# Optimization experiments

Hardware: AMD Instinct MI355X
Metric: run time of the kernel (lower is better)

The kernel has to match this reference:

```python
import jax, jax.numpy as jnp
import numpy as np

N_NODES = 100000
N_EDGES = 3200000
IN_DIM, H_DIM, OUT_DIM = 512, 256, 128
NEG_SLOPE = 0.25


def setup_inputs() -> dict:
    key = jax.random.key(0)
    ks = jax.random.split(key, 8)
    x = jax.random.normal(ks[0], (N_NODES, IN_DIM), dtype=jnp.float32)
    # xavier-normal-ish init for weights, zero bias (matches module init)
    W1 = jax.random.normal(ks[1], (IN_DIM, H_DIM), dtype=jnp.float32) * np.sqrt(2.0 / (IN_DIM + H_DIM))
    b1 = jnp.zeros((H_DIM,), dtype=jnp.float32)
    W2 = jax.random.normal(ks[2], (H_DIM, OUT_DIM), dtype=jnp.float32) * np.sqrt(2.0 / (H_DIM + OUT_DIM))
    b2 = jnp.zeros((OUT_DIM,), dtype=jnp.float32)
    adj_row = jax.random.randint(ks[3], (N_EDGES,), 0, N_NODES, dtype=jnp.int32)
    adj_col = jax.random.randint(ks[4], (N_EDGES,), 0, N_NODES, dtype=jnp.int32)
    # positive normalized-ish edge weights (like D^-1/2 A D^-1/2 entries)
    edge_weight = jax.random.uniform(ks[5], (N_EDGES,), dtype=jnp.float32) * 0.05
    return {"x": x, "W1": W1, "b1": b1, "W2": W2, "b2": b2,
            "adj_row": adj_row, "adj_col": adj_col, "edge_weight": edge_weight}


def reference(x, W1, b1, W2, b2, adj_row, adj_col, edge_weight):
    n = x.shape[0]

    def spmm(support):
        # out[r] = sum over edges (r, c): w * support[c]   (COO SpMM)
        msgs = edge_weight[:, None] * support[adj_col]  # [E, d] gather
        return jax.ops.segment_sum(msgs, adj_row, num_segments=n)

    def leaky(h):
        return jnp.where(h > 0, h, NEG_SLOPE * h)

    h = leaky(spmm(x @ W1) + b1)          # gc1 + leaky_relu (dropout = eval mode)
    h = leaky(spmm(h @ W2) + b2)          # gc2 + leaky_relu
    return h
```

## Files before the change

### kernel.cpp

```cpp
#include <hip/hip_runtime.h>

typedef unsigned short u16;
typedef unsigned char u8;
typedef __attribute__((ext_vector_type(8))) __bf16 bf16x8;
typedef __attribute__((ext_vector_type(4))) float f32x4;

#define CAP   4608
#define CHUNK 8192
#define NBKT_PAD 800

static __device__ __forceinline__ u16 f2bf(float f) {
    unsigned u = __float_as_uint(f);
    u += 0x7fffu + ((u >> 16) & 1u);
    return (u16)(u >> 16);
}
static __device__ __forceinline__ float bf2f(u16 v) {
    return __uint_as_float(((unsigned)v) << 16);
}
static __device__ __forceinline__ void gl_lds16(const void* g, void* l) {
    __builtin_amdgcn_global_load_lds((const __attribute__((address_space(1))) void*)g,
                                     (__attribute__((address_space(3))) void*)l, 16, 0, 0);
}


__global__ __launch_bounds__(256) void bucket_k(const int* __restrict__ row,
                                                const int* __restrict__ col,
                                                const float* __restrict__ w,
                                                int* __restrict__ gcount,
                                                int2* __restrict__ edges, int E) {
    __shared__ int hist[NBKT_PAD];
    __shared__ int lscan[NBKT_PAD];
    __shared__ int lcnt[NBKT_PAD];
    __shared__ int gbase[NBKT_PAD];
    __shared__ int tsum[256];
    __shared__ int2 pay[CHUNK];
    __shared__ int  dst[CHUNK];
    const int base = blockIdx.x * CHUNK;
    const int cntC = min(CHUNK, E - base);
    const int tid = threadIdx.x;

    for (int i = tid; i < NBKT_PAD; i += 256) { hist[i] = 0; lcnt[i] = 0; }
    __syncthreads();

    for (int i = tid; i < cntC; i += 256) atomicAdd(&hist[row[base + i] >> 7], 1);
    __syncthreads();

    int h[4], s = 0;
    #pragma unroll
    for (int j = 0; j < 4; ++j) {
        int bb = tid * 4 + j;
        h[j] = (bb < NBKT_PAD) ? hist[bb] : 0;
        s += h[j];
    }
    tsum[tid] = s;
    __syncthreads();
    for (int d = 1; d < 256; d <<= 1) {
        int t = (tid >= d) ? tsum[tid - d] : 0;
        __syncthreads();
        tsum[tid] += t;
        __syncthreads();
    }
    int run = tsum[tid] - s;
    #pragma unroll
    for (int j = 0; j < 4; ++j) {
        int bb = tid * 4 + j;
        if (bb < NBKT_PAD) {
            lscan[bb] = run;
            run += h[j];
            if (h[j] > 0) gbase[bb] = atomicAdd(&gcount[bb], h[j]);
        }
    }
    __syncthreads();

    for (int i = tid; i < cntC; i += 256) {
        int r = row[base + i];
        int c = col[base + i];
        float ww = w[base + i];
        int bb = r >> 7;
        int lp = atomicAdd(&lcnt[bb], 1);
        int slot = lscan[bb] + lp;
        int pos = gbase[bb] + lp;
        pay[slot] = make_int2(((r & 127) << 17) | c, __float_as_int(ww));
        dst[slot] = (pos < CAP) ? bb * CAP + pos : -1;
    }
    __syncthreads();

    for (int i = tid; i < cntC; i += 256) {
        int d = dst[i];
        if (d >= 0) edges[d] = pay[i];
    }
}


__global__ __launch_bounds__(256) void rsort_k(const int* __restrict__ gcount,
                                               int2* __restrict__ edges,
                                               int2* __restrict__ rc, int n) {
    __shared__ int2 pay[CAP];
    __shared__ int2 pay2[CAP];
    __shared__ int hist[128];
    __shared__ int sc[128];
    __shared__ int lcnt[128];
    const int b = blockIdx.x, tid = threadIdx.x;
    const int cnt = min(gcount[b], CAP);
    int2* eb = edges + (size_t)b * CAP;

    if (tid < 128) { hist[tid] = 0; lcnt[tid] = 0; }
    __syncthreads();

    for (int i = tid; i < cnt; i += 256) {
        int2 e = eb[i];
        pay[i] = e;
        atomicAdd(&hist[((unsigned)e.x) >> 17], 1);
    }
    __syncthreads();

    int h = (tid < 128) ? hist[tid] : 0;
    if (tid < 128) sc[tid] = h;
    __syncthreads();
    for (int d = 1; d < 128; d <<= 1) {
        int t = 0;
        if (tid < 128 && tid >= d) t = sc[tid - d];
        __syncthreads();
        if (tid < 128) sc[tid] += t;
        __syncthreads();
    }
    if (tid < 128) {
        sc[tid] -= h;
        int gr = b * 128 + tid;
        if (gr < n) rc[gr] = make_int2(b * CAP + sc[tid], h);
    }
    __syncthreads();

    for (int i = tid; i < cnt; i += 256) {
        int2 e = pay[i];
        int rr = ((unsigned)e.x) >> 17;
        int slot = sc[rr] + atomicAdd(&lcnt[rr], 1);
        pay2[slot] = e;
    }
    __syncthreads();

    for (int i = tid; i < cnt; i += 256) eb[i] = pay2[i];
}


__global__ __launch_bounds__(256) void cvt_x(const float* __restrict__ x,
                                             u16* __restrict__ xb, long total) {
    long i = ((long)blockIdx.x * 256 + threadIdx.x) * 8;
    const long stride = (long)gridDim.x * 2048;
    for (; i < total; i += stride) {
        float4 f0 = *(const float4*)(x + i);
        float4 f1 = *(const float4*)(x + i + 4);
        alignas(16) u16 t[8];
        t[0] = f2bf(f0.x); t[1] = f2bf(f0.y); t[2] = f2bf(f0.z); t[3] = f2bf(f0.w);
        t[4] = f2bf(f1.x); t[5] = f2bf(f1.y); t[6] = f2bf(f1.z); t[7] = f2bf(f1.w);
        *(int4*)(xb + i) = *(const int4*)t;
    }
}


__global__ void transpose_w2(const float* __restrict__ W1, u16* __restrict__ W1T,
                             const float* __restrict__ W2, u16* __restrict__ W2T) {
    const int T1 = 512 * 256;
    const int T2 = 256 * 128;
    int i = blockIdx.x * blockDim.x + threadIdx.x;
    if (i < T1) {
        int k = i / 256, nn = i % 256;
        W1T[nn * 512 + k] = f2bf(W1[i]);
    } else if (i < T1 + T2) {
        int j = i - T1;
        int k = j / 128, nn = j % 128;
        W2T[nn * 256 + k] = f2bf(W2[j]);
    }
}


template <int K, int NWN>
__global__ void gemm_fq(const u16* __restrict__ A,
                        const u16* __restrict__ BT,
                        u8* __restrict__ supq,
                        float* __restrict__ scales, int M) {
    constexpr int BN = NWN * 64;
    constexpr int THREADS = NWN * 128;
    constexpr int A_ISS = 8192 / (THREADS * 16);
    constexpr int B_ISS = (BN * 64) / (THREADS * 16);
    constexpr int LOGN = (NWN == 4) ? 2 : 1;
    __shared__ alignas(16) u16 As[128 * 32];
    __shared__ alignas(16) u16 Bs[BN * 32];
    __shared__ float rmax[128][NWN];
    __shared__ u8 qtile[128 * BN];

    const int tid = threadIdx.x;
    const int lane = tid & 63, wv = tid >> 6;
    const int wm = wv >> LOGN, wn = wv & (NWN - 1);
    const int lr = lane & 15, lg = lane >> 4;
    const int mblk = blockIdx.x;
    f32x4 acc[4][4] = {};

    const u16* gA[A_ISS];
    const u16* gB[B_ISS];
    u16* lA[A_ISS];
    u16* lB[B_ISS];
    #pragma unroll
    for (int i = 0; i < A_ISS; ++i) {
        int t8 = i * THREADS + tid;
        long r = (long)mblk * 128 + (t8 >> 2);
        if (r >= M) r = M - 1;
        gA[i] = A + r * K + (t8 & 3) * 8;
        lA[i] = As + i * THREADS * 8 + wv * 512;
    }
    #pragma unroll
    for (int i = 0; i < B_ISS; ++i) {
        int t8 = i * THREADS + tid;
        gB[i] = BT + (long)(t8 >> 2) * K + (t8 & 3) * 8;
        lB[i] = Bs + i * THREADS * 8 + wv * 512;
    }

    #pragma unroll 2
    for (int kt = 0; kt < K; kt += 32) {
        #pragma unroll
        for (int i = 0; i < A_ISS; ++i) gl_lds16(gA[i] + kt, lA[i]);
        #pragma unroll
        for (int i = 0; i < B_ISS; ++i) gl_lds16(gB[i] + kt, lB[i]);
        __syncthreads();

        bf16x8 a[4], b[4];
        #pragma unroll
        for (int mi = 0; mi < 4; ++mi)
            a[mi] = *(const bf16x8*)&As[(wm * 64 + mi * 16 + lr) * 32 + lg * 8];
        #pragma unroll
        for (int ni = 0; ni < 4; ++ni)
            b[ni] = *(const bf16x8*)&Bs[(wn * 64 + ni * 16 + lr) * 32 + lg * 8];
        #pragma unroll
        for (int mi = 0; mi < 4; ++mi)
            #pragma unroll
            for (int ni = 0; ni < 4; ++ni)
                acc[mi][ni] = __builtin_amdgcn_mfma_f32_16x16x32_bf16(a[mi], b[ni], acc[mi][ni], 0, 0, 0);
        __syncthreads();
    }

    #pragma unroll
    for (int mi = 0; mi < 4; ++mi) {
        #pragma unroll
        for (int j = 0; j < 4; ++j) {
            float m = 0.f;
            #pragma unroll
            for (int ni = 0; ni < 4; ++ni) m = fmaxf(m, fabsf(acc[mi][ni][j]));
            m = fmaxf(m, __shfl_xor(m, 1));
            m = fmaxf(m, __shfl_xor(m, 2));
            m = fmaxf(m, __shfl_xor(m, 4));
            m = fmaxf(m, __shfl_xor(m, 8));
            if (lr == 0) rmax[wm * 64 + mi * 16 + lg * 4 + j][wn] = m;
        }
    }
    __syncthreads();

    #pragma unroll
    for (int mi = 0; mi < 4; ++mi) {
        #pragma unroll
        for (int j = 0; j < 4; ++j) {
            const int rl = wm * 64 + mi * 16 + lg * 4 + j;
            float m = rmax[rl][0];
            #pragma unroll
            for (int w2 = 1; w2 < NWN; ++w2) m = fmaxf(m, rmax[rl][w2]);
            const float inv = (m > 0.f) ? 127.f / m : 0.f;
            #pragma unroll
            for (int ni = 0; ni < 4; ++ni) {
                int q = (int)rintf(acc[mi][ni][j] * inv) + 128;
                qtile[rl * BN + wn * 64 + ni * 16 + lr] = (u8)q;
            }
        }
    }
    if (tid < 128) {
        int gr = mblk * 128 + tid;
        if (gr < M) {
            float m = rmax[tid][0];
            #pragma unroll
            for (int w2 = 1; w2 < NWN; ++w2) m = fmaxf(m, rmax[tid][w2]);
            scales[gr] = m * (1.f / 127.f);
        }
    }
    __syncthreads();

    constexpr int CHUNKS = (128 * BN) / (THREADS * 16);
    #pragma unroll
    for (int cc = 0; cc < CHUNKS; ++cc) {
        int off = cc * THREADS * 16 + tid * 16;
        int gr = mblk * 128 + off / BN;
        if (gr < M)
            *(int4*)(supq + (size_t)mblk * 128 * BN + off) = *(const int4*)&qtile[off];
    }
}


template <int D, bool OUT_BF16>
__global__ __launch_bounds__(256) void spmm_q(const int2* __restrict__ rc,
                                              const int2* __restrict__ edges,
                                              const u8* __restrict__ supq,
                                              const float* __restrict__ scales,
                                              const float* __restrict__ bias,
                                              u16* __restrict__ obf,
                                              float* __restrict__ of32, int n) {
    const int r = blockIdx.x * 4 + (threadIdx.x >> 6);
    if (r >= n) return;
    const int lane = threadIdx.x & 63;
    constexpr int V = D / 64;
    float acc[V];
    #pragma unroll
    for (int j = 0; j < V; ++j) acc[j] = 0.f;
    float kk = 0.f;

    const int2 se0 = rc[r];
    const int e0  = __builtin_amdgcn_readfirstlane(se0.x);
    const int cnt = __builtin_amdgcn_readfirstlane(se0.y);
    const int2* __restrict__ eb = edges + e0;
    const int loff = lane * V;

    int i = 0;
    for (; i + 4 <= cnt; i += 4) {
        int2 e[4];
        #pragma unroll
        for (int j = 0; j < 4; ++j) e[j] = eb[i + j];
        int c[4], sw[4];
        #pragma unroll
        for (int j = 0; j < 4; ++j) {
            c[j]  = __builtin_amdgcn_readfirstlane(e[j].x) & 0x1FFFF;
            sw[j] = __builtin_amdgcn_readfirstlane(e[j].y);
        }
        float s[4];
        #pragma unroll
        for (int j = 0; j < 4; ++j) s[j] = scales[c[j]];
        unsigned uv[4];
        #pragma unroll
        for (int j = 0; j < 4; ++j)
            uv[j] = *(const unsigned*)(supq + (size_t)c[j] * D + loff);
        float ws[4];
        #pragma unroll
        for (int j = 0; j < 4; ++j) ws[j] = __int_as_float(sw[j]) * s[j];
        #pragma unroll
        for (int j = 0; j < 4; ++j) {
            kk += ws[j];
            acc[0] += ws[j] * (float)(uv[j] & 0xFF);
            acc[1] += ws[j] * (float)((uv[j] >> 8) & 0xFF);
            if constexpr (V == 4) {
                acc[2] += ws[j] * (float)((uv[j] >> 16) & 0xFF);
                acc[3] += ws[j] * (float)(uv[j] >> 24);
            }
        }
    }
    for (; i < cnt; ++i) {
        int2 e = eb[i];
        int c  = __builtin_amdgcn_readfirstlane(e.x) & 0x1FFFF;
        int sw = __builtin_amdgcn_readfirstlane(e.y);
        float ws = __int_as_float(sw) * scales[c];
        unsigned uv = *(const unsigned*)(supq + (size_t)c * D + loff);
        kk += ws;
        acc[0] += ws * (float)(uv & 0xFF);
        acc[1] += ws * (float)((uv >> 8) & 0xFF);
        if constexpr (V == 4) {
            acc[2] += ws * (float)((uv >> 16) & 0xFF);
            acc[3] += ws * (float)(uv >> 24);
        }
    }

    const float off = 128.f * kk;
    if constexpr (V == 4) {
        const float4 bb = *(const float4*)&bias[lane * 4];
        float h0 = acc[0] - off + bb.x, h1 = acc[1] - off + bb.y;
        float h2 = acc[2] - off + bb.z, h3 = acc[3] - off + bb.w;
        h0 = h0 > 0.f ? h0 : 0.25f * h0;
        h1 = h1 > 0.f ? h1 : 0.25f * h1;
        h2 = h2 > 0.f ? h2 : 0.25f * h2;
        h3 = h3 > 0.f ? h3 : 0.25f * h3;
        const size_t o = (size_t)r * D + lane * 4;
        if constexpr (OUT_BF16) {
            ushort4 hv; hv.x = f2bf(h0); hv.y = f2bf(h1); hv.z = f2bf(h2); hv.w = f2bf(h3);
            *(ushort4*)&obf[o] = hv;
        } else {
            *(float4*)&of32[o] = make_float4(h0, h1, h2, h3);
        }
    } else {
        const float2 bb = *(const float2*)&bias[lane * 2];
        float h0 = acc[0] - off + bb.x, h1 = acc[1] - off + bb.y;
        h0 = h0 > 0.f ? h0 : 0.25f * h0;
        h1 = h1 > 0.f ? h1 : 0.25f * h1;
        const size_t o = (size_t)r * D + lane * 2;
        if constexpr (OUT_BF16) {
            ushort2 hv; hv.x = f2bf(h0); hv.y = f2bf(h1);
            *(ushort2*)&obf[o] = hv;
        } else {
            *(float2*)&of32[o] = make_float2(h0, h1);
        }
    }
}


extern "C" void kernel_launch(void* const* d_in, const int* in_sizes, int n_in,
                              void* d_out, int out_size, void* d_ws, size_t ws_size,
                              hipStream_t stream) {
    const float* x  = (const float*)d_in[0];
    const float* W1 = (const float*)d_in[1];
    const float* b1 = (const float*)d_in[2];
    const float* W2 = (const float*)d_in[3];
    const float* b2 = (const float*)d_in[4];
    const int* arow = (const int*)d_in[5];
    const int* acol = (const int*)d_in[6];
    const float* ew = (const float*)d_in[7];

    const int IN = 512, H = 256, OUT = 128;
    const int n = in_sizes[0] / IN;
    const int E = in_sizes[5];
    const int nbkt = (n + 127) >> 7;

    char* base = (char*)d_ws;
    size_t off = 0;
    auto carve = [&](size_t bytes) -> void* {
        void* r = base + off;
        off = (off + bytes + 255) & ~(size_t)255;
        return r;
    };
    int*   gcount = (int*)carve((size_t)NBKT_PAD * 4);
    int2*  edges  = (int2*)carve((size_t)nbkt * CAP * 8);
    int2*  rc     = (int2*)carve((size_t)n * 8);
    u16*   W1T    = (u16*)carve((size_t)H * IN * 2);
    u16*   W2T    = (u16*)carve((size_t)OUT * H * 2);
    u8*    supq   = (u8*)carve((size_t)n * H);
    float* scales = (float*)carve((size_t)n * 4);
    u16*   xb     = (u16*)carve((size_t)n * IN * 2);
    u16*   h1     = xb;

    hipMemsetAsync(gcount, 0, (size_t)NBKT_PAD * 4, stream);
    bucket_k<<<(E + CHUNK - 1) / CHUNK, 256, 0, stream>>>(arow, acol, ew, gcount, edges, E);
    rsort_k<<<nbkt, 256, 0, stream>>>(gcount, edges, rc, n);

    transpose_w2<<<(512 * 256 + 256 * 128 + 255) / 256, 256, 0, stream>>>(W1, W1T, W2, W2T);
    cvt_x<<<2048, 256, 0, stream>>>(x, xb, (long)n * IN);

    gemm_fq<512, 4><<<(n + 127) / 128, 512, 0, stream>>>(xb, W1T, supq, scales, n);
    spmm_q<256, true><<<(n + 3) / 4, 256, 0, stream>>>(rc, edges, supq, scales, b1, h1, nullptr, n);

    gemm_fq<256, 2><<<(n + 127) / 128, 256, 0, stream>>>(h1, W2T, supq, scales, n);
    spmm_q<128, false><<<(n + 3) / 4, 256, 0, stream>>>(rc, edges, supq, scales, b2, nullptr, (float*)d_out, n);
}
```

Before: 506.6 us.

## Split edges into SoA column-banded CSR, prescale weights, fuse x conversion into GEMM

The row-sort kernel now orders each row's edges by column band and writes separate column and weight arrays, padding each row to a multiple of four with zero-weight edges. A new pass multiplies each edge weight by the per-node quantization scale, so the SpMM does vector loads of four edges and software-pipelines its gathers without a dependent scale lookup. The standalone fp32-to-bf16 conversion of x is removed: the first GEMM now loads fp32 A tiles directly and converts them in registers. The costs are extra pre-scale kernels, padded storage, and register-path A loads in the GEMM in place of direct global-to-LDS loads.

```diff
diff --git a/kernel.cpp b/kernel.cpp
--- a/kernel.cpp
+++ b/kernel.cpp
@@ -6,8 +6,10 @@
 typedef __attribute__((ext_vector_type(4))) float f32x4;
 
 #define CAP   4608
+#define CAPO  5120
 #define CHUNK 8192
 #define NBKT_PAD 800
+#define NBAND 32
 
 static __device__ __forceinline__ u16 f2bf(float f) {
     unsigned u = __float_as_uint(f);
@@ -93,29 +95,38 @@
 
 
 __global__ __launch_bounds__(256) void rsort_k(const int* __restrict__ gcount,
-                                               int2* __restrict__ edges,
+                                               const int2* __restrict__ edges,
+                                               int* __restrict__ colsO,
+                                               float* __restrict__ wO,
                                                int2* __restrict__ rc, int n) {
-    __shared__ int2 pay[CAP];
-    __shared__ int2 pay2[CAP];
-    __shared__ int hist[128];
+    __shared__ int cnt2[128 * NBAND];
+    __shared__ int base2[128 * NBAND];
+    __shared__ int colsL[CAPO];
+    __shared__ float wL[CAPO];
     __shared__ int sc[128];
-    __shared__ int lcnt[128];
     const int b = blockIdx.x, tid = threadIdx.x;
     const int cnt = min(gcount[b], CAP);
-    int2* eb = edges + (size_t)b * CAP;
-
-    if (tid < 128) { hist[tid] = 0; lcnt[tid] = 0; }
+    const int2* eb = edges + (size_t)b * CAP;
+
+    for (int i = tid; i < 128 * NBAND; i += 256) cnt2[i] = 0;
+    for (int i = tid; i < CAPO; i += 256) { colsL[i] = 0; wL[i] = 0.f; }
     __syncthreads();
 
     for (int i = tid; i < cnt; i += 256) {
         int2 e = eb[i];
-        pay[i] = e;
-        atomicAdd(&hist[((unsigned)e.x) >> 17], 1);
-    }
-    __syncthreads();
-
-    int h = (tid < 128) ? hist[tid] : 0;
-    if (tid < 128) sc[tid] = h;
+        int rr = ((unsigned)e.x) >> 17;
+        int cc = e.x & 0x1FFFF;
+        atomicAdd(&cnt2[rr * NBAND + (cc >> 12)], 1);
+    }
+    __syncthreads();
+
+    int rtot = 0;
+    if (tid < 128) {
+        #pragma unroll
+        for (int bb = 0; bb < NBAND; ++bb) rtot += cnt2[tid * NBAND + bb];
+        rtot = (rtot + 3) & ~3;
+        sc[tid] = rtot;
+    }
     __syncthreads();
     for (int d = 1; d < 128; d <<= 1) {
         int t = 0;
@@ -125,35 +136,49 @@
         __syncthreads();
     }
     if (tid < 128) {
-        sc[tid] -= h;
+        int start = sc[tid] - rtot;
         int gr = b * 128 + tid;
-        if (gr < n) rc[gr] = make_int2(b * CAP + sc[tid], h);
+        if (gr < n) rc[gr] = make_int2(b * CAPO + start, rtot);
+        int run = start;
+        #pragma unroll
+        for (int bb = 0; bb < NBAND; ++bb) {
+            base2[tid * NBAND + bb] = run;
+            run += cnt2[tid * NBAND + bb];
+        }
     }
     __syncthreads();
 
     for (int i = tid; i < cnt; i += 256) {
-        int2 e = pay[i];
+        int2 e = eb[i];
         int rr = ((unsigned)e.x) >> 17;
-        int slot = sc[rr] + atomicAdd(&lcnt[rr], 1);
-        pay2[slot] = e;
-    }
-    __syncthreads();
-
-    for (int i = tid; i < cnt; i += 256) eb[i] = pay2[i];
-}
-
-
-__global__ __launch_bounds__(256) void cvt_x(const float* __restrict__ x,
-                                             u16* __restrict__ xb, long total) {
-    long i = ((long)blockIdx.x * 256 + threadIdx.x) * 8;
-    const long stride = (long)gridDim.x * 2048;
+        int cc = e.x & 0x1FFFF;
+        int slot = atomicAdd(&base2[rr * NBAND + (cc >> 12)], 1);
+        colsL[slot] = cc;
+        wL[slot] = __int_as_float(e.y);
+    }
+    __syncthreads();
+
+    int* co = colsO + (size_t)b * CAPO;
+    float* wo = wO + (size_t)b * CAPO;
+    for (int i = tid; i < CAPO; i += 256) { co[i] = colsL[i]; wo[i] = wL[i]; }
+}
+
+
+__global__ __launch_bounds__(256) void wscale_k(const int* __restrict__ cols,
+                                                const float* __restrict__ wr,
+                                                const float* __restrict__ scales,
+                                                float* __restrict__ ws, int total) {
+    int i = (blockIdx.x * 256 + threadIdx.x) * 4;
+    const int stride = gridDim.x * 1024;
     for (; i < total; i += stride) {
-        float4 f0 = *(const float4*)(x + i);
-        float4 f1 = *(const float4*)(x + i + 4);
-        alignas(16) u16 t[8];
-        t[0] = f2bf(f0.x); t[1] = f2bf(f0.y); t[2] = f2bf(f0.z); t[3] = f2bf(f0.w);
-        t[4] = f2bf(f1.x); t[5] = f2bf(f1.y); t[6] = f2bf(f1.z); t[7] = f2bf(f1.w);
-        *(int4*)(xb + i) = *(const int4*)t;
+        int4 c = *(const int4*)(cols + i);
+        float4 w = *(const float4*)(wr + i);
+        float4 o;
+        o.x = w.x * scales[c.x];
+        o.y = w.y * scales[c.y];
+        o.z = w.z * scales[c.z];
+        o.w = w.w * scales[c.w];
+        *(float4*)(ws + i) = o;
     }
 }
 
@@ -174,8 +199,8 @@
 }
 
 
-template <int K, int NWN>
-__global__ void gemm_fq(const u16* __restrict__ A,
+template <int K, int NWN, bool AF32>
+__global__ void gemm_fq(const void* __restrict__ Ap,
                         const u16* __restrict__ BT,
                         u8* __restrict__ supq,
                         float* __restrict__ scales, int M) {
@@ -183,6 +208,7 @@
     constexpr int THREADS = NWN * 128;
     constexpr int A_ISS = 8192 / (THREADS * 16);
     constexpr int B_ISS = (BN * 64) / (THREADS * 16);
+    constexpr int A_CH = 4096 / (THREADS * 8);
     constexpr int LOGN = (NWN == 4) ? 2 : 1;
     __shared__ alignas(16) u16 As[128 * 32];
     __shared__ alignas(16) u16 Bs[BN * 32];
@@ -195,19 +221,34 @@
     const int lr = lane & 15, lg = lane >> 4;
     const int mblk = blockIdx.x;
     f32x4 acc[4][4] = {};
-
-    const u16* gA[A_ISS];
+    const float* Af = (const float*)Ap;
+    const u16* Ab = (const u16*)Ap;
+
+    const u16* gA[A_ISS > 0 ? A_ISS : 1];
+    u16* lA[A_ISS > 0 ? A_ISS : 1];
+    const float* gAf[A_CH > 0 ? A_CH : 1];
+    u16* lAf[A_CH > 0 ? A_CH : 1];
+    if constexpr (AF32) {
+        #pragma unroll
+        for (int i = 0; i < A_CH; ++i) {
+            int t8 = i * THREADS + tid;
+            long r = (long)mblk * 128 + (t8 >> 2);
+            if (r >= M) r = M - 1;
+            gAf[i] = Af + r * K + (t8 & 3) * 8;
+            lAf[i] = As + (t8 >> 2) * 32 + (t8 & 3) * 8;
+        }
+    } else {
+        #pragma unroll
+        for (int i = 0; i < A_ISS; ++i) {
+            int t8 = i * THREADS + tid;
+            long r = (long)mblk * 128 + (t8 >> 2);
+            if (r >= M) r = M - 1;
+            gA[i] = Ab + r * K + (t8 & 3) * 8;
+            lA[i] = As + i * THREADS * 8 + wv * 512;
+        }
+    }
     const u16* gB[B_ISS];
-    u16* lA[A_ISS];
     u16* lB[B_ISS];
-    #pragma unroll
-    for (int i = 0; i < A_ISS; ++i) {
-        int t8 = i * THREADS + tid;
-        long r = (long)mblk * 128 + (t8 >> 2);
-        if (r >= M) r = M - 1;
-        gA[i] = A + r * K + (t8 & 3) * 8;
-        lA[i] = As + i * THREADS * 8 + wv * 512;
-    }
     #pragma unroll
     for (int i = 0; i < B_ISS; ++i) {
         int t8 = i * THREADS + tid;
@@ -217,8 +258,20 @@
 
     #pragma unroll 2
     for (int kt = 0; kt < K; kt += 32) {
-        #pragma unroll
-        for (int i = 0; i < A_ISS; ++i) gl_lds16(gA[i] + kt, lA[i]);
+        if constexpr (AF32) {
+            #pragma unroll
+            for (int i = 0; i < A_CH; ++i) {
+                float4 f0 = *(const float4*)(gAf[i] + kt);
+                float4 f1 = *(const float4*)(gAf[i] + kt + 4);
+                alignas(16) u16 t[8];
+                t[0] = f2bf(f0.x); t[1] = f2bf(f0.y); t[2] = f2bf(f0.z); t[3] = f2bf(f0.w);
+                t[4] = f2bf(f1.x); t[5] = f2bf(f1.y); t[6] = f2bf(f1.z); t[7] = f2bf(f1.w);
+                *(int4*)lAf[i] = *(const int4*)t;
+            }
+        } else {
+            #pragma unroll
+            for (int i = 0; i < A_ISS; ++i) gl_lds16(gA[i] + kt, lA[i]);
+        }
         #pragma unroll
         for (int i = 0; i < B_ISS; ++i) gl_lds16(gB[i] + kt, lB[i]);
         __syncthreads();
@@ -293,10 +346,10 @@
 
 
 template <int D, bool OUT_BF16>
-__global__ __launch_bounds__(256) void spmm_q(const int2* __restrict__ rc,
-                                              const int2* __restrict__ edges,
+__global__ __launch_bounds__(256) void spmm_p(const int2* __restrict__ rc,
+                                              const int* __restrict__ cols,
+                                              const float* __restrict__ ws,
                                               const u8* __restrict__ supq,
-                                              const float* __restrict__ scales,
                                               const float* __restrict__ bias,
                                               u16* __restrict__ obf,
                                               float* __restrict__ of32, int n) {
@@ -309,58 +362,55 @@
     for (int j = 0; j < V; ++j) acc[j] = 0.f;
     float kk = 0.f;
 
-    const int2 se0 = rc[r];
-    const int e0  = __builtin_amdgcn_readfirstlane(se0.x);
-    const int cnt = __builtin_amdgcn_readfirstlane(se0.y);
-    const int2* __restrict__ eb = edges + e0;
+    const int2 se = rc[r];
+    const int e0  = __builtin_amdgcn_readfirstlane(se.x);
+    const int cnt = __builtin_amdgcn_readfirstlane(se.y);
+    const int* __restrict__ cp = cols + e0;
+    const float* __restrict__ wp = ws + e0;
     const int loff = lane * V;
 
-    int i = 0;
-    for (; i + 4 <= cnt; i += 4) {
-        int2 e[4];
-        #pragma unroll
-        for (int j = 0; j < 4; ++j) e[j] = eb[i + j];
-        int c[4], sw[4];
-        #pragma unroll
-        for (int j = 0; j < 4; ++j) {
-            c[j]  = __builtin_amdgcn_readfirstlane(e[j].x) & 0x1FFFF;
-            sw[j] = __builtin_amdgcn_readfirstlane(e[j].y);
-        }
-        float s[4];
-        #pragma unroll
-        for (int j = 0; j < 4; ++j) s[j] = scales[c[j]];
-        unsigned uv[4];
-        #pragma unroll
-        for (int j = 0; j < 4; ++j)
-            uv[j] = *(const unsigned*)(supq + (size_t)c[j] * D + loff);
-        float ws[4];
-        #pragma unroll
-        for (int j = 0; j < 4; ++j) ws[j] = __int_as_float(sw[j]) * s[j];
-        #pragma unroll
-        for (int j = 0; j < 4; ++j) {
-            kk += ws[j];
-            acc[0] += ws[j] * (float)(uv[j] & 0xFF);
-            acc[1] += ws[j] * (float)((uv[j] >> 8) & 0xFF);
+    #define GATH(dst, c)                                                        \
+        if constexpr (V == 4) dst = *(const unsigned*)(supq + (c) * D + loff);  \
+        else                  dst = *(const u16*)(supq + (c) * D + loff);
+
+    if (cnt > 0) {
+        int4 c0 = *(const int4*)cp;
+        float4 w0 = *(const float4*)wp;
+        unsigned g0, g1, g2, g3;
+        GATH(g0, c0.x); GATH(g1, c0.y); GATH(g2, c0.z); GATH(g3, c0.w);
+        int i = 4;
+        while (i < cnt) {
+            int4 c1 = *(const int4*)(cp + i);
+            float4 w1 = *(const float4*)(wp + i);
+            unsigned h0, h1, h2, h3;
+            GATH(h0, c1.x); GATH(h1, c1.y); GATH(h2, c1.z); GATH(h3, c1.w);
+            kk += w0.x + w0.y + w0.z + w0.w;
+            acc[0] += w0.x * (float)(g0 & 0xFF) + w0.y * (float)(g1 & 0xFF)
+                    + w0.z * (float)(g2 & 0xFF) + w0.w * (float)(g3 & 0xFF);
+            acc[1] += w0.x * (float)((g0 >> 8) & 0xFF) + w0.y * (float)((g1 >> 8) & 0xFF)
+                    + w0.z * (float)((g2 >> 8) & 0xFF) + w0.w * (float)((g3 >> 8) & 0xFF);
             if constexpr (V == 4) {
-                acc[2] += ws[j] * (float)((uv[j] >> 16) & 0xFF);
-                acc[3] += ws[j] * (float)(uv[j] >> 24);
+                acc[2] += w0.x * (float)((g0 >> 16) & 0xFF) + w0.y * (float)((g1 >> 16) & 0xFF)
+                        + w0.z * (float)((g2 >> 16) & 0xFF) + w0.w * (float)((g3 >> 16) & 0xFF);
+                acc[3] += w0.x * (float)(g0 >> 24) + w0.y * (float)(g1 >> 24)
+                        + w0.z * (float)(g2 >> 24) + w0.w * (float)(g3 >> 24);
             }
-        }
-    }
-    for (; i < cnt; ++i) {
-        int2 e = eb[i];
-        int c  = __builtin_amdgcn_readfirstlane(e.x) & 0x1FFFF;
-        int sw = __builtin_amdgcn_readfirstlane(e.y);
-        float ws = __int_as_float(sw) * scales[c];
-        unsigned uv = *(const unsigned*)(supq + (size_t)c * D + loff);
-        kk += ws;
-        acc[0] += ws * (float)(uv & 0xFF);
-        acc[1] += ws * (float)((uv >> 8) & 0xFF);
+            c0 = c1; w0 = w1; g0 = h0; g1 = h1; g2 = h2; g3 = h3;
+            i += 4;
+        }
+        kk += w0.x + w0.y + w0.z + w0.w;
+        acc[0] += w0.x * (float)(g0 & 0xFF) + w0.y * (float)(g1 & 0xFF)
+                + w0.z * (float)(g2 & 0xFF) + w0.w * (float)(g3 & 0xFF);
+        acc[1] += w0.x * (float)((g0 >> 8) & 0xFF) + w0.y * (float)((g1 >> 8) & 0xFF)
+                + w0.z * (float)((g2 >> 8) & 0xFF) + w0.w * (float)((g3 >> 8) & 0xFF);
         if constexpr (V == 4) {
-            acc[2] += ws * (float)((uv >> 16) & 0xFF);
-            acc[3] += ws * (float)(uv >> 24);
-        }
-    }
+            acc[2] += w0.x * (float)((g0 >> 16) & 0xFF) + w0.y * (float)((g1 >> 16) & 0xFF)
+                    + w0.z * (float)((g2 >> 16) & 0xFF) + w0.w * (float)((g3 >> 16) & 0xFF);
+            acc[3] += w0.x * (float)(g0 >> 24) + w0.y * (float)(g1 >> 24)
+                    + w0.z * (float)(g2 >> 24) + w0.w * (float)(g3 >> 24);
+        }
+    }
+    #undef GATH
 
     const float off = 128.f * kk;
     if constexpr (V == 4) {
@@ -410,6 +460,7 @@
     const int n = in_sizes[0] / IN;
     const int E = in_sizes[5];
     const int nbkt = (n + 127) >> 7;
+    const int totS = nbkt * CAPO;
 
     char* base = (char*)d_ws;
     size_t off = 0;
@@ -420,24 +471,27 @@
     };
     int*   gcount = (int*)carve((size_t)NBKT_PAD * 4);
     int2*  edges  = (int2*)carve((size_t)nbkt * CAP * 8);
+    int*   colsS  = (int*)carve((size_t)totS * 4);
+    float* wraw   = (float*)carve((size_t)totS * 4);
+    float* wsS    = (float*)carve((size_t)totS * 4);
     int2*  rc     = (int2*)carve((size_t)n * 8);
     u16*   W1T    = (u16*)carve((size_t)H * IN * 2);
     u16*   W2T    = (u16*)carve((size_t)OUT * H * 2);
     u8*    supq   = (u8*)carve((size_t)n * H);
     float* scales = (float*)carve((size_t)n * 4);
-    u16*   xb     = (u16*)carve((size_t)n * IN * 2);
-    u16*   h1     = xb;
+    u16*   h1     = (u16*)carve((size_t)n * H * 2);
 
     hipMemsetAsync(gcount, 0, (size_t)NBKT_PAD * 4, stream);
     bucket_k<<<(E + CHUNK - 1) / CHUNK, 256, 0, stream>>>(arow, acol, ew, gcount, edges, E);
-    rsort_k<<<nbkt, 256, 0, stream>>>(gcount, edges, rc, n);
+    rsort_k<<<nbkt, 256, 0, stream>>>(gcount, edges, colsS, wraw, rc, n);
 
     transpose_w2<<<(512 * 256 + 256 * 128 + 255) / 256, 256, 0, stream>>>(W1, W1T, W2, W2T);
-    cvt_x<<<2048, 256, 0, stream>>>(x, xb, (long)n * IN);
-
-    gemm_fq<512, 4><<<(n + 127) / 128, 512, 0, stream>>>(xb, W1T, supq, scales, n);
-    spmm_q<256, true><<<(n + 3) / 4, 256, 0, stream>>>(rc, edges, supq, scales, b1, h1, nullptr, n);
-
-    gemm_fq<256, 2><<<(n + 127) / 128, 256, 0, stream>>>(h1, W2T, supq, scales, n);
-    spmm_q<128, false><<<(n + 3) / 4, 256, 0, stream>>>(rc, edges, supq, scales, b2, nullptr, (float*)d_out, n);
-}
+
+    gemm_fq<512, 4, true><<<(n + 127) / 128, 512, 0, stream>>>(x, W1T, supq, scales, n);
+    wscale_k<<<(totS / 4 + 255) / 256, 256, 0, stream>>>(colsS, wraw, scales, wsS, totS);
+    spmm_p<256, true><<<(n + 3) / 4, 256, 0, stream>>>(rc, colsS, wsS, supq, b1, h1, nullptr, n);
+
+    gemm_fq<256, 2, false><<<(n + 127) / 128, 256, 0, stream>>>(h1, W2T, supq, scales, n);
+    wscale_k<<<(totS / 4 + 255) / 256, 256, 0, stream>>>(colsS, wraw, scales, wsS, totS);
+    spmm_p<128, false><<<(n + 3) / 4, 256, 0, stream>>>(rc, colsS, wsS, supq, b2, nullptr, (float*)d_out, n);
+}
```

Result: faster. 455.0 us (-10.2%).
